# Performance work log

Hardware: AMD Instinct MI355X
Metric: run time of the kernel (lower is better)

Reference implementation:

```python
import jax, jax.numpy as jnp
import numpy as np

B, T = 64, 2048
D_RNN, D_EMB, D_ATT = 1024, 512, 128
N_FILT, KSIZE = 32, 31
PAD = (KSIZE - 1) // 2


def setup_inputs() -> dict:
    key = jax.random.key(0)
    ks = jax.random.split(key, 9)
    return {
        "attention_hidden_state": jax.random.normal(ks[0], (B, D_RNN), jnp.float32),
        "memory": jax.random.normal(ks[1], (B, T, D_EMB), jnp.float32),
        "processed_memory": jax.random.normal(ks[2], (B, T, D_ATT), jnp.float32),
        "attention_weights_cat": jax.random.uniform(ks[3], (B, 2, T), jnp.float32),
        "mask": jax.random.randint(ks[4], (B, T), 0, 2) > 0,
        # learned params (all bias-free, as in the torch module)
        "Wq": jax.random.normal(ks[5], (D_ATT, D_RNN), jnp.float32) * 0.02,   # query_layer.weight
        "Wv": jax.random.normal(ks[6], (1, D_ATT), jnp.float32) * 0.02,        # v.weight
        "conv_w": jax.random.normal(ks[7], (N_FILT, 2, KSIZE), jnp.float32) * 0.1,  # location_conv.weight (OIH)
        "Wd": jax.random.normal(ks[8], (D_ATT, N_FILT), jnp.float32) * 0.02,   # location_dense.weight
    }


def reference(attention_hidden_state, memory, processed_memory,
              attention_weights_cat, mask, Wq, Wv, conv_w, Wd):
    # processed query: [B, 1, D_ATT]
    pq = (attention_hidden_state @ Wq.T)[:, None, :]
    # location features: Conv1d(2 -> N_FILT, same padding) over time
    loc = jax.lax.conv_general_dilated(
        attention_weights_cat, conv_w,
        window_strides=(1,), padding=[(PAD, PAD)],
        dimension_numbers=("NCH", "OIH", "NCH"))           # [B, N_FILT, T]
    paw = jnp.einsum("bft,af->bta", loc, Wd)               # [B, T, D_ATT]
    # additive energies -> scalar per position via v-projection
    energies = jnp.einsum("bta,a->bt", jnp.tanh(pq + paw + processed_memory), Wv[0])
    alignment = jnp.where(mask, -jnp.inf, energies)         # masked fill
    attention_weights = jax.nn.softmax(alignment, axis=1)   # [B, T]
    attention_context = jnp.einsum("bt,btd->bd", attention_weights, memory)  # [B, D_EMB]
    return attention_context, jax.lax.stop_gradient(attention_weights)
```

## Files before the change

kernel.cpp:

```cpp
#include <hip/hip_runtime.h>
#include <math.h>

#define B_    64
#define T_    2048
#define DRNN  1024
#define DEMB  512
#define DATT  128
#define NF    32
#define KS    31
#define PADL  15
#define TT    32
#define CT    64
#define NC    (T_/CT)

__device__ __forceinline__ float fast_tanh(float x){
    float e2 = __expf(2.0f * x);
    return 1.0f - 2.0f / (e2 + 1.0f);
}

__global__ __launch_bounds__(512) void prep_kernel(
    const float* __restrict__ hidden, const float* __restrict__ Wq,
    const float* __restrict__ Wd, const float* __restrict__ convw,
    float* __restrict__ pq, float* __restrict__ M2)
{
    const int blk = blockIdx.x;
    const int tid = threadIdx.x;
    if (blk < B_) {
        const int b    = blk;
        const int lane = tid & 63;
        const int w    = tid >> 6;
        float4 h[4];
        #pragma unroll
        for (int j = 0; j < 4; ++j)
            h[j] = *(const float4*)(hidden + b*DRNN + lane*4 + j*256);
        for (int ai = 0; ai < 16; ++ai){
            const int a = w*16 + ai;
            const float4* wq4 = (const float4*)(Wq + (size_t)a*DRNN);
            float acc = 0.f;
            #pragma unroll
            for (int j = 0; j < 4; ++j){
                const float4 q = wq4[lane + j*64];
                acc = fmaf(q.x, h[j].x, acc);
                acc = fmaf(q.y, h[j].y, acc);
                acc = fmaf(q.z, h[j].z, acc);
                acc = fmaf(q.w, h[j].w, acc);
            }
            acc += __shfl_xor(acc, 1, 64);  acc += __shfl_xor(acc, 2, 64);
            acc += __shfl_xor(acc, 4, 64);  acc += __shfl_xor(acc, 8, 64);
            acc += __shfl_xor(acc, 16, 64); acc += __shfl_xor(acc, 32, 64);
            if (lane == 0) pq[b*DATT + a] = acc;
        }
    } else {
        const int a = tid & 127;
        const int g = tid >> 7;
        float wd[NF];
        #pragma unroll
        for (int f = 0; f < NF; ++f) wd[f] = Wd[a*NF + f];
        const int cklo = g*16;
        const int ckhi = (g*16 + 16 < 2*KS) ? (g*16 + 16) : 2*KS;
        for (int ck = cklo; ck < ckhi; ++ck){
            float acc = 0.f;
            #pragma unroll
            for (int f = 0; f < NF; ++f) acc = fmaf(wd[f], convw[f*2*KS + ck], acc);
            M2[ck*DATT + a] = acc;
        }
    }
}

__global__ __launch_bounds__(256, 4) void fused_kernel(
    const float* __restrict__ pm, const float* __restrict__ awcat,
    const float* __restrict__ pq, const float* __restrict__ M2,
    const float* __restrict__ Wv, const int* __restrict__ mask,
    const float* __restrict__ memory,
    float* __restrict__ pbuf, float* __restrict__ pmax,
    float* __restrict__ psum, float* __restrict__ pctx)
{
    const int b   = blockIdx.y;
    const int cx  = blockIdx.x;
    const int t0  = cx * CT;
    const int tid = threadIdx.x;
    const int s   = tid >> 7;
    const int a   = tid & 127;
    const int ts  = t0 + TT * s;
    const int lane = tid & 63;

    __shared__ float saw0[96], saw1[96];
    __shared__ float sred[2][2][TT];
    __shared__ float2 swt[CT];
    __shared__ int   scount;
    __shared__ float4 sacc[128];
    __shared__ unsigned int smkbits[2];

    int mymk = 0;
    if (lane < 32) mymk = (mask[b*T_ + ts + lane] != 0);
    const unsigned long long bal0 = __ballot(mymk);
    const unsigned mkb = (unsigned)bal0;

    const float pqa = pq[b*DATT + a];
    const float wv  = Wv[a];
    const float* pmb = pm + ((size_t)(b*T_ + ts)) * DATT + a;
    float acc[TT];
    #pragma unroll
    for (int t = 0; t < TT; ++t){
        acc[t] = 0.f;
        if (((mkb >> t) & 1u) == 0u) acc[t] = pmb[(size_t)t * DATT];
    }
    float Ma0[KS], Ma1[KS];
    const float* M2a = M2 + a;
    #pragma unroll
    for (int k = 0; k < KS; ++k){
        Ma0[k] = M2a[(size_t)k * DATT];
        Ma1[k] = M2a[(size_t)(KS + k) * DATT];
    }

    for (int i = tid; i < 94; i += 256){
        int tt = t0 - PADL + i;
        bool ok = (tt >= 0) && (tt < T_);
        saw0[i] = ok ? awcat[(b*2+0)*T_ + tt] : 0.f;
        saw1[i] = ok ? awcat[(b*2+1)*T_ + tt] : 0.f;
    }
    if (tid < 64){
        const int mk = mask[b*T_ + t0 + tid] != 0;
        const unsigned long long bal = __ballot(mk);
        if (tid == 0){
            smkbits[0] = (unsigned)bal;
            smkbits[1] = (unsigned)(bal >> 32);
        }
    }
    __syncthreads();

    #pragma unroll
    for (int t = 0; t < TT; ++t) acc[t] += pqa;

    #pragma unroll
    for (int j = 0; j < TT + KS - 1; ++j){
        const float av0 = saw0[j + TT*s];
        const float av1 = saw1[j + TT*s];
        const int tlo = (j - KS + 1) > 0 ? (j - KS + 1) : 0;
        const int thi = (j < TT - 1) ? j : (TT - 1);
        #pragma unroll
        for (int t = tlo; t <= thi; ++t){
            acc[t] = fmaf(Ma0[j - t], av0, acc[t]);
            acc[t] = fmaf(Ma1[j - t], av1, acc[t]);
        }
    }

    #pragma unroll
    for (int t = 0; t < TT; ++t){
        acc[t] = wv * fast_tanh(acc[t]);
    }

    const int half = a >> 6;
    #pragma unroll
    for (int k = 0; k < 16; ++k){
        const bool hi = (lane & 1) != 0;
        float send = hi ? acc[k] : acc[k+16];
        float recv = __shfl_xor(send, 1, 64);
        acc[k] = (hi ? acc[k+16] : acc[k]) + recv;
    }
    #pragma unroll
    for (int k = 0; k < 8; ++k){
        const bool hi = (lane & 2) != 0;
        float send = hi ? acc[k] : acc[k+8];
        float recv = __shfl_xor(send, 2, 64);
        acc[k] = (hi ? acc[k+8] : acc[k]) + recv;
    }
    #pragma unroll
    for (int k = 0; k < 4; ++k){
        const bool hi = (lane & 4) != 0;
        float send = hi ? acc[k] : acc[k+4];
        float recv = __shfl_xor(send, 4, 64);
        acc[k] = (hi ? acc[k+4] : acc[k]) + recv;
    }
    #pragma unroll
    for (int k = 0; k < 2; ++k){
        const bool hi = (lane & 8) != 0;
        float send = hi ? acc[k] : acc[k+2];
        float recv = __shfl_xor(send, 8, 64);
        acc[k] = (hi ? acc[k+2] : acc[k]) + recv;
    }
    {
        const bool hi = (lane & 16) != 0;
        float send = hi ? acc[0] : acc[1];
        float recv = __shfl_xor(send, 16, 64);
        acc[0] = (hi ? acc[1] : acc[0]) + recv;
    }
    acc[0] += __shfl_xor(acc[0], 32, 64);
    const int trev = ((lane & 1) << 4) | (((lane >> 1) & 1) << 3) |
                     (((lane >> 2) & 1) << 2) | (((lane >> 3) & 1) << 1) |
                     ((lane >> 4) & 1);
    if (lane < 32) sred[s][half][trev] = acc[0];
    __syncthreads();

    if (tid < 64){
        const int t = t0 + tid;
        float e = sred[tid>>5][0][tid&31] + sred[tid>>5][1][tid&31];
        const int mk = (smkbits[tid>>5] >> (tid&31)) & 1u;
        float mval = mk ? -1e30f : e;
        #pragma unroll
        for (int off = 1; off < 64; off <<= 1) mval = fmaxf(mval, __shfl_xor(mval, off, 64));
        const float pval = mk ? 0.f : __expf(e - mval);
        float sv = pval;
        #pragma unroll
        for (int off = 1; off < 64; off <<= 1) sv += __shfl_xor(sv, off, 64);
        pbuf[b*T_ + t] = pval;
        const unsigned long long bal = __ballot(pval != 0.f);
        if (pval != 0.f){
            const int pfx = (int)__popcll(bal & ((1ull << tid) - 1ull));
            swt[pfx] = make_float2(pval, __int_as_float(tid));
        }
        if (tid == 0){
            scount = (int)__popcll(bal);
            pmax[b*NC + cx] = mval;
            psum[b*NC + cx] = sv;
        }
    }
    __syncthreads();

    const int n   = scount;
    const int col = tid & 127;
    const int row = tid >> 7;
    float4 a4 = make_float4(0.f, 0.f, 0.f, 0.f);
    const float4* mem4 = (const float4*)memory + ((size_t)(b*T_ + t0))*(DEMB/4) + col;

    int i = row;
    for (; i + 6 < n; i += 8){
        const float2 e0 = swt[i];
        const float2 e1 = swt[i+2];
        const float2 e2 = swt[i+4];
        const float2 e3 = swt[i+6];
        const float4 m0 = mem4[(size_t)__float_as_int(e0.y) * (DEMB/4)];
        const float4 m1 = mem4[(size_t)__float_as_int(e1.y) * (DEMB/4)];
        const float4 m2 = mem4[(size_t)__float_as_int(e2.y) * (DEMB/4)];
        const float4 m3 = mem4[(size_t)__float_as_int(e3.y) * (DEMB/4)];
        a4.x = fmaf(e0.x, m0.x, a4.x); a4.y = fmaf(e0.x, m0.y, a4.y);
        a4.z = fmaf(e0.x, m0.z, a4.z); a4.w = fmaf(e0.x, m0.w, a4.w);
        a4.x = fmaf(e1.x, m1.x, a4.x); a4.y = fmaf(e1.x, m1.y, a4.y);
        a4.z = fmaf(e1.x, m1.z, a4.z); a4.w = fmaf(e1.x, m1.w, a4.w);
        a4.x = fmaf(e2.x, m2.x, a4.x); a4.y = fmaf(e2.x, m2.y, a4.y);
        a4.z = fmaf(e2.x, m2.z, a4.z); a4.w = fmaf(e2.x, m2.w, a4.w);
        a4.x = fmaf(e3.x, m3.x, a4.x); a4.y = fmaf(e3.x, m3.y, a4.y);
        a4.z = fmaf(e3.x, m3.z, a4.z); a4.w = fmaf(e3.x, m3.w, a4.w);
    }
    for (; i < n; i += 2){
        const float2 e = swt[i];
        const float4 m = mem4[(size_t)__float_as_int(e.y) * (DEMB/4)];
        a4.x = fmaf(e.x, m.x, a4.x); a4.y = fmaf(e.x, m.y, a4.y);
        a4.z = fmaf(e.x, m.z, a4.z); a4.w = fmaf(e.x, m.w, a4.w);
    }

    if (row == 1) sacc[col] = a4;
    __syncthreads();
    if (row == 0){
        const float4 o = sacc[col];
        float4* dst = (float4*)(pctx + ((size_t)(b*NC + cx))*DEMB) + col;
        *dst = make_float4(a4.x + o.x, a4.y + o.y, a4.z + o.z, a4.w + o.w);
    }
}

__global__ __launch_bounds__(256) void finalize_kernel(
    const float* __restrict__ pbuf, const float* __restrict__ pmax,
    const float* __restrict__ psum, const float* __restrict__ pctx,
    float* __restrict__ ctx, float* __restrict__ wout)
{
    const int b   = blockIdx.y;
    const int g   = blockIdx.x;
    const int tid = threadIdx.x;
    __shared__ float sscale[NC];

    if (tid < 64){
        float mv = (tid < NC) ? pmax[b*NC + tid] : -1e30f;
        float sv = (tid < NC) ? psum[b*NC + tid] : 0.f;
        float gm = mv;
        #pragma unroll
        for (int off = 1; off < 64; off <<= 1) gm = fmaxf(gm, __shfl_xor(gm, off, 64));
        float z = sv * __expf(mv - gm);
        #pragma unroll
        for (int off = 1; off < 64; off <<= 1) z += __shfl_xor(z, off, 64);
        if (tid < NC) sscale[tid] = __expf(mv - gm) / z;
    }
    __syncthreads();

    if (g == 0){
        float2 a2 = make_float2(0.f, 0.f);
        const float2* pc2 = (const float2*)(pctx + (size_t)b*NC*DEMB) + tid;
        #pragma unroll
        for (int c = 0; c < NC; ++c){
            const float sc = sscale[c];
            const float2 v = pc2[(size_t)c * (DEMB/2)];
            a2.x = fmaf(sc, v.x, a2.x);
            a2.y = fmaf(sc, v.y, a2.y);
        }
        ((float2*)(ctx + b*DEMB))[tid] = a2;
    }

    const int t = g*256 + tid;
    wout[b*T_ + t] = pbuf[b*T_ + t] * sscale[t >> 6];
}

extern "C" void kernel_launch(void* const* d_in, const int* in_sizes, int n_in,
                              void* d_out, int out_size, void* d_ws, size_t ws_size,
                              hipStream_t stream)
{
    const float* hidden = (const float*)d_in[0];
    const float* memory = (const float*)d_in[1];
    const float* pm     = (const float*)d_in[2];
    const float* awcat  = (const float*)d_in[3];
    const int*   mask   = (const int*)d_in[4];
    const float* Wq     = (const float*)d_in[5];
    const float* Wv     = (const float*)d_in[6];
    const float* convw  = (const float*)d_in[7];
    const float* Wd     = (const float*)d_in[8];

    float* out  = (float*)d_out;
    float* ctx  = out;
    float* wout = out + B_*DEMB;

    float* pq    = (float*)d_ws;
    float* M2    = pq   + B_*DATT;
    float* pbuf  = M2   + 8192;
    float* pmax  = pbuf + B_*T_;
    float* psum  = pmax + B_*NC;
    float* pctx  = psum + B_*NC;

    prep_kernel<<<dim3(B_ + 1), 512, 0, stream>>>(hidden, Wq, Wd, convw, pq, M2);
    fused_kernel<<<dim3(NC, B_), 256, 0, stream>>>(pm, awcat, pq, M2, Wv, mask,
                                                   memory, pbuf, pmax, psum, pctx);
    finalize_kernel<<<dim3(8, B_), 256, 0, stream>>>(pbuf, pmax, psum, pctx, ctx, wout);
}
```

Before: 405.0 us.

## Split conv into two channel passes and replace shared-memory compaction with wave-local bitmask

The location conv now runs one input channel at a time, so only 31 conv weights are held in registers instead of 62. The occupancy hint is raised from 4 to 5 blocks per CU. Each wave loads its own attention-weight window into shared memory, and every wave redundantly computes the chunk softmax stats. Nonzero positions are then taken from a ballot bitmask with ctz and shuffles instead of a shared-memory compaction, which removes one of the block barriers. The cost is duplicated softmax and mask loads per wave, a second pass over the accumulators, and a serial ctz-based tail loop.

```diff
diff --git a/kernel.cpp b/kernel.cpp
--- a/kernel.cpp
+++ b/kernel.cpp
@@ -12,6 +12,7 @@
 #define TT    32
 #define CT    64
 #define NC    (T_/CT)
+#define DEMB4 (DEMB/4)
 
 __device__ __forceinline__ float fast_tanh(float x){
     float e2 = __expf(2.0f * x);
@@ -67,7 +68,7 @@
     }
 }
 
-__global__ __launch_bounds__(256, 4) void fused_kernel(
+__global__ __launch_bounds__(256, 5) void fused_kernel(
     const float* __restrict__ pm, const float* __restrict__ awcat,
     const float* __restrict__ pq, const float* __restrict__ M2,
     const float* __restrict__ Wv, const int* __restrict__ mask,
@@ -75,29 +76,24 @@
     float* __restrict__ pbuf, float* __restrict__ pmax,
     float* __restrict__ psum, float* __restrict__ pctx)
 {
-    const int b   = blockIdx.y;
-    const int cx  = blockIdx.x;
-    const int t0  = cx * CT;
-    const int tid = threadIdx.x;
-    const int s   = tid >> 7;
-    const int a   = tid & 127;
-    const int ts  = t0 + TT * s;
+    const int b    = blockIdx.y;
+    const int cx   = blockIdx.x;
+    const int t0   = cx * CT;
+    const int tid  = threadIdx.x;
+    const int wvi  = tid >> 6;
     const int lane = tid & 63;
-
-    __shared__ float saw0[96], saw1[96];
+    const int s    = tid >> 7;
+    const int a    = tid & 127;
+    const int ts   = t0 + TT * s;
+
+    __shared__ float sawW[4][2][64];
     __shared__ float sred[2][2][TT];
-    __shared__ float2 swt[CT];
-    __shared__ int   scount;
     __shared__ float4 sacc[128];
-    __shared__ unsigned int smkbits[2];
 
     int mymk = 0;
     if (lane < 32) mymk = (mask[b*T_ + ts + lane] != 0);
-    const unsigned long long bal0 = __ballot(mymk);
-    const unsigned mkb = (unsigned)bal0;
-
-    const float pqa = pq[b*DATT + a];
-    const float wv  = Wv[a];
+    const unsigned mkb = (unsigned)__ballot(mymk);
+
     const float* pmb = pm + ((size_t)(b*T_ + ts)) * DATT + a;
     float acc[TT];
     #pragma unroll
@@ -105,50 +101,47 @@
         acc[t] = 0.f;
         if (((mkb >> t) & 1u) == 0u) acc[t] = pmb[(size_t)t * DATT];
     }
-    float Ma0[KS], Ma1[KS];
+
+    {
+        const int tt = ts - PADL + lane;
+        const bool ok = (tt >= 0) && (tt < T_) && (lane < 62);
+        sawW[wvi][0][lane] = ok ? awcat[(b*2+0)*T_ + tt] : 0.f;
+        sawW[wvi][1][lane] = ok ? awcat[(b*2+1)*T_ + tt] : 0.f;
+    }
+
+    const float pqa = pq[b*DATT + a];
+    const float wvv = Wv[a];
+    #pragma unroll
+    for (int t = 0; t < TT; ++t) acc[t] += pqa;
+
+    float Ma[KS];
     const float* M2a = M2 + a;
     #pragma unroll
-    for (int k = 0; k < KS; ++k){
-        Ma0[k] = M2a[(size_t)k * DATT];
-        Ma1[k] = M2a[(size_t)(KS + k) * DATT];
-    }
-
-    for (int i = tid; i < 94; i += 256){
-        int tt = t0 - PADL + i;
-        bool ok = (tt >= 0) && (tt < T_);
-        saw0[i] = ok ? awcat[(b*2+0)*T_ + tt] : 0.f;
-        saw1[i] = ok ? awcat[(b*2+1)*T_ + tt] : 0.f;
-    }
-    if (tid < 64){
-        const int mk = mask[b*T_ + t0 + tid] != 0;
-        const unsigned long long bal = __ballot(mk);
-        if (tid == 0){
-            smkbits[0] = (unsigned)bal;
-            smkbits[1] = (unsigned)(bal >> 32);
-        }
-    }
-    __syncthreads();
-
-    #pragma unroll
-    for (int t = 0; t < TT; ++t) acc[t] += pqa;
-
+    for (int k = 0; k < KS; ++k) Ma[k] = M2a[(size_t)k * DATT];
     #pragma unroll
     for (int j = 0; j < TT + KS - 1; ++j){
-        const float av0 = saw0[j + TT*s];
-        const float av1 = saw1[j + TT*s];
+        const float av = sawW[wvi][0][j];
         const int tlo = (j - KS + 1) > 0 ? (j - KS + 1) : 0;
         const int thi = (j < TT - 1) ? j : (TT - 1);
         #pragma unroll
-        for (int t = tlo; t <= thi; ++t){
-            acc[t] = fmaf(Ma0[j - t], av0, acc[t]);
-            acc[t] = fmaf(Ma1[j - t], av1, acc[t]);
-        }
-    }
-
-    #pragma unroll
-    for (int t = 0; t < TT; ++t){
-        acc[t] = wv * fast_tanh(acc[t]);
-    }
+        for (int t = tlo; t <= thi; ++t)
+            acc[t] = fmaf(Ma[j - t], av, acc[t]);
+    }
+    asm volatile("" ::: "memory");
+    #pragma unroll
+    for (int k = 0; k < KS; ++k) Ma[k] = M2a[(size_t)(KS + k) * DATT];
+    #pragma unroll
+    for (int j = 0; j < TT + KS - 1; ++j){
+        const float av = sawW[wvi][1][j];
+        const int tlo = (j - KS + 1) > 0 ? (j - KS + 1) : 0;
+        const int thi = (j < TT - 1) ? j : (TT - 1);
+        #pragma unroll
+        for (int t = tlo; t <= thi; ++t)
+            acc[t] = fmaf(Ma[j - t], av, acc[t]);
+    }
+
+    #pragma unroll
+    for (int t = 0; t < TT; ++t) acc[t] = wvv * fast_tanh(acc[t]);
 
     const int half = a >> 6;
     #pragma unroll
@@ -192,61 +185,67 @@
     if (lane < 32) sred[s][half][trev] = acc[0];
     __syncthreads();
 
-    if (tid < 64){
-        const int t = t0 + tid;
-        float e = sred[tid>>5][0][tid&31] + sred[tid>>5][1][tid&31];
-        const int mk = (smkbits[tid>>5] >> (tid&31)) & 1u;
-        float mval = mk ? -1e30f : e;
-        #pragma unroll
-        for (int off = 1; off < 64; off <<= 1) mval = fmaxf(mval, __shfl_xor(mval, off, 64));
-        const float pval = mk ? 0.f : __expf(e - mval);
-        float sv = pval;
-        #pragma unroll
-        for (int off = 1; off < 64; off <<= 1) sv += __shfl_xor(sv, off, 64);
-        pbuf[b*T_ + t] = pval;
-        const unsigned long long bal = __ballot(pval != 0.f);
-        if (pval != 0.f){
-            const int pfx = (int)__popcll(bal & ((1ull << tid) - 1ull));
-            swt[pfx] = make_float2(pval, __int_as_float(tid));
-        }
-        if (tid == 0){
-            scount = (int)__popcll(bal);
+    const int tme = t0 + lane;
+    float e = sred[lane>>5][0][lane&31] + sred[lane>>5][1][lane&31];
+    const int mk2 = (mask[b*T_ + tme] != 0);
+    float mval = mk2 ? -1e30f : e;
+    #pragma unroll
+    for (int off = 1; off < 64; off <<= 1) mval = fmaxf(mval, __shfl_xor(mval, off, 64));
+    const float pval = mk2 ? 0.f : __expf(e - mval);
+    float sv = pval;
+    #pragma unroll
+    for (int off = 1; off < 64; off <<= 1) sv += __shfl_xor(sv, off, 64);
+    const unsigned long long bal = __ballot(pval != 0.f);
+    const int n = (int)__popcll(bal);
+    if (wvi == 0){
+        pbuf[b*T_ + tme] = pval;
+        if (lane == 0){
             pmax[b*NC + cx] = mval;
             psum[b*NC + cx] = sv;
         }
     }
-    __syncthreads();
-
-    const int n   = scount;
+
     const int col = tid & 127;
     const int row = tid >> 7;
     float4 a4 = make_float4(0.f, 0.f, 0.f, 0.f);
-    const float4* mem4 = (const float4*)memory + ((size_t)(b*T_ + t0))*(DEMB/4) + col;
-
-    int i = row;
-    for (; i + 6 < n; i += 8){
-        const float2 e0 = swt[i];
-        const float2 e1 = swt[i+2];
-        const float2 e2 = swt[i+4];
-        const float2 e3 = swt[i+6];
-        const float4 m0 = mem4[(size_t)__float_as_int(e0.y) * (DEMB/4)];
-        const float4 m1 = mem4[(size_t)__float_as_int(e1.y) * (DEMB/4)];
-        const float4 m2 = mem4[(size_t)__float_as_int(e2.y) * (DEMB/4)];
-        const float4 m3 = mem4[(size_t)__float_as_int(e3.y) * (DEMB/4)];
-        a4.x = fmaf(e0.x, m0.x, a4.x); a4.y = fmaf(e0.x, m0.y, a4.y);
-        a4.z = fmaf(e0.x, m0.z, a4.z); a4.w = fmaf(e0.x, m0.w, a4.w);
-        a4.x = fmaf(e1.x, m1.x, a4.x); a4.y = fmaf(e1.x, m1.y, a4.y);
-        a4.z = fmaf(e1.x, m1.z, a4.z); a4.w = fmaf(e1.x, m1.w, a4.w);
-        a4.x = fmaf(e2.x, m2.x, a4.x); a4.y = fmaf(e2.x, m2.y, a4.y);
-        a4.z = fmaf(e2.x, m2.z, a4.z); a4.w = fmaf(e2.x, m2.w, a4.w);
-        a4.x = fmaf(e3.x, m3.x, a4.x); a4.y = fmaf(e3.x, m3.y, a4.y);
-        a4.z = fmaf(e3.x, m3.z, a4.z); a4.w = fmaf(e3.x, m3.w, a4.w);
-    }
-    for (; i < n; i += 2){
-        const float2 e = swt[i];
-        const float4 m = mem4[(size_t)__float_as_int(e.y) * (DEMB/4)];
-        a4.x = fmaf(e.x, m.x, a4.x); a4.y = fmaf(e.x, m.y, a4.y);
-        a4.z = fmaf(e.x, m.z, a4.z); a4.w = fmaf(e.x, m.w, a4.w);
+    const float4* mem4 = (const float4*)memory + ((size_t)(b*T_ + t0))*DEMB4 + col;
+
+    unsigned long long mbits = bal;
+    int i = 0;
+    for (; i + 8 <= n; i += 8){
+        int tb[8];
+        #pragma unroll
+        for (int u = 0; u < 8; ++u){
+            tb[u] = (int)__builtin_ctzll(mbits);
+            mbits &= mbits - 1ull;
+        }
+        const int i0 = tb[row+0], i1 = tb[row+2], i2 = tb[row+4], i3 = tb[row+6];
+        const float p0 = __shfl(pval, i0, 64);
+        const float p1 = __shfl(pval, i1, 64);
+        const float p2 = __shfl(pval, i2, 64);
+        const float p3 = __shfl(pval, i3, 64);
+        const float4 m0 = mem4[(size_t)i0 * DEMB4];
+        const float4 m1 = mem4[(size_t)i1 * DEMB4];
+        const float4 m2 = mem4[(size_t)i2 * DEMB4];
+        const float4 m3 = mem4[(size_t)i3 * DEMB4];
+        a4.x = fmaf(p0, m0.x, a4.x); a4.y = fmaf(p0, m0.y, a4.y);
+        a4.z = fmaf(p0, m0.z, a4.z); a4.w = fmaf(p0, m0.w, a4.w);
+        a4.x = fmaf(p1, m1.x, a4.x); a4.y = fmaf(p1, m1.y, a4.y);
+        a4.z = fmaf(p1, m1.z, a4.z); a4.w = fmaf(p1, m1.w, a4.w);
+        a4.x = fmaf(p2, m2.x, a4.x); a4.y = fmaf(p2, m2.y, a4.y);
+        a4.z = fmaf(p2, m2.z, a4.z); a4.w = fmaf(p2, m2.w, a4.w);
+        a4.x = fmaf(p3, m3.x, a4.x); a4.y = fmaf(p3, m3.y, a4.y);
+        a4.z = fmaf(p3, m3.z, a4.z); a4.w = fmaf(p3, m3.w, a4.w);
+    }
+    for (; i < n; ++i){
+        const int tb = (int)__builtin_ctzll(mbits);
+        mbits &= mbits - 1ull;
+        if ((i & 1) == row){
+            const float p = __shfl(pval, tb, 64);
+            const float4 m = mem4[(size_t)tb * DEMB4];
+            a4.x = fmaf(p, m.x, a4.x); a4.y = fmaf(p, m.y, a4.y);
+            a4.z = fmaf(p, m.z, a4.z); a4.w = fmaf(p, m.w, a4.w);
+        }
     }
 
     if (row == 1) sacc[col] = a4;
```

After: 413.2 us. 2.0% more time.
